# Optimization experiments

Hardware: AMD Instinct MI355X
Metric: run time of the kernel (lower is better)

The kernel has to match this reference:

```python
import jax, jax.numpy as jnp
import numpy as np
import math

D_MODEL = 2048
D_STATE = 64
D_CONV = 4
EXPAND = 2
HEADDIM = 128
NGROUPS = 1
CHUNK = 256
D_INNER = EXPAND * D_MODEL            # 4096
NHEADS = D_INNER // HEADDIM           # 32
CONV_DIM = D_INNER + 2 * NGROUPS * D_STATE   # 4224
D_IN_PROJ = 2 * D_INNER + 2 * NGROUPS * D_STATE + NHEADS  # 8352
BATCH, SEQLEN = 2, 4096
EPS = 1e-5


def segsum(x):
    # x: (..., T) -> (..., T, T) with s[i, j] = sum_{k=j+1}^{i} x[k], -inf above diag
    T = x.shape[-1]
    xx = jnp.broadcast_to(x[..., :, None], x.shape + (T,))
    mask_lo = jnp.tril(jnp.ones((T, T), dtype=bool), -1)
    xx = jnp.where(mask_lo, xx, 0.0)
    s = jnp.cumsum(xx, axis=-2)
    mask = jnp.tril(jnp.ones((T, T), dtype=bool), 0)
    return jnp.where(mask, s, -jnp.inf)


def ssd(X, A, B, C, block_len):
    # X:(b,L,h,p)  A:(b,L,h)  B,C:(b,L,h,n)
    b, L, h, p = X.shape
    c = L // block_len
    X = X.reshape(b, c, block_len, h, p)
    A = A.reshape(b, c, block_len, h).transpose(0, 3, 1, 2)  # b h c l
    B = B.reshape(b, c, block_len, h, -1)
    C = C.reshape(b, c, block_len, h, -1)
    A_cumsum = jnp.cumsum(A, axis=-1)
    Lmat = jnp.exp(segsum(A))                                  # b h c l l
    Y_diag = jnp.einsum('bclhn,bcshn,bhcls,bcshp->bclhp', C, B, Lmat, X)
    decay_states = jnp.exp(A_cumsum[:, :, :, -1:] - A_cumsum)  # b h c l
    states = jnp.einsum('bclhn,bhcl,bclhp->bchpn', B, decay_states, X)
    init = jnp.zeros_like(states[:, :1])
    states = jnp.concatenate([init, states], axis=1)
    decay_chunk = jnp.exp(segsum(jnp.pad(A_cumsum[:, :, :, -1], ((0, 0), (0, 0), (1, 0)))))
    new_states = jnp.einsum('bhzc,bchpn->bzhpn', decay_chunk, states)
    states, final_state = new_states[:, :-1], new_states[:, -1]
    Y_off = jnp.einsum('bclhn,bchpn,bhcl->bclhp', C, states, jnp.exp(A_cumsum))
    Y = (Y_diag + Y_off).reshape(b, L, h, p)
    return Y, final_state


def causal_dwconv(x, w, b):
    # x:(B,L,C)  w:(C,K) depthwise kernel  b:(C,)  -> causal conv, length preserved
    C, K = w.shape
    y = jax.lax.conv_general_dilated(
        x.transpose(0, 2, 1), w[:, None, :], (1,), [(K - 1, 0)],
        feature_group_count=C)
    return y.transpose(0, 2, 1) + b


def setup_inputs() -> dict:
    key = jax.random.key(0)
    ks = jax.random.split(key, 8)
    u = jax.random.normal(ks[0], (BATCH, SEQLEN, D_MODEL), dtype=jnp.float32)
    W_in = jax.random.normal(ks[1], (D_MODEL, D_IN_PROJ), dtype=jnp.float32) / np.sqrt(D_MODEL)
    conv_w = jax.random.normal(ks[2], (CONV_DIM, D_CONV), dtype=jnp.float32) / np.sqrt(D_CONV)
    conv_b = jnp.zeros((CONV_DIM,), dtype=jnp.float32)
    # dt_bias init: inverse-softplus of dt sampled log-uniform in [dt_min, dt_max]
    dt_min, dt_max, dt_floor = 1e-3, 1e-1, 1e-4
    dt = jnp.exp(jax.random.uniform(ks[3], (NHEADS,)) * (math.log(dt_max) - math.log(dt_min)) + math.log(dt_min))
    dt = jnp.clip(dt, dt_floor)
    dt_bias = dt + jnp.log(-jnp.expm1(-dt))
    A_log = jnp.log(jax.random.uniform(ks[4], (NHEADS,), minval=1.0, maxval=16.0))
    D = jnp.ones((NHEADS,), dtype=jnp.float32)
    norm_w = jnp.ones((D_INNER,), dtype=jnp.float32)
    W_out = jax.random.normal(ks[5], (D_INNER, D_MODEL), dtype=jnp.float32) / np.sqrt(D_INNER)
    return {"u": u, "W_in": W_in, "conv_w": conv_w, "conv_b": conv_b,
            "dt_bias": dt_bias, "A_log": A_log, "D": D, "norm_w": norm_w, "W_out": W_out}


def reference(u, W_in, conv_w, conv_b, dt_bias, A_log, D, norm_w, W_out):
    batch, seqlen, _ = u.shape
    zxbcdt = u @ W_in                                   # (B,L,8352)
    z, xBC, dt = jnp.split(zxbcdt, [D_INNER, D_INNER + CONV_DIM], axis=-1)
    dt = jax.nn.softplus(dt + dt_bias)                  # (B,L,H)
    xBC = jax.nn.silu(causal_dwconv(xBC, conv_w, conv_b))
    x, B, C = jnp.split(xBC, [D_INNER, D_INNER + NGROUPS * D_STATE], axis=-1)
    x = x.reshape(batch, seqlen, NHEADS, HEADDIM)
    B = jnp.broadcast_to(B.reshape(batch, seqlen, NGROUPS, D_STATE), (batch, seqlen, NHEADS, D_STATE))
    C = jnp.broadcast_to(C.reshape(batch, seqlen, NGROUPS, D_STATE), (batch, seqlen, NHEADS, D_STATE))
    A = -jnp.exp(A_log)                                 # (H,)
    x_scaled = x * dt[..., None]
    A_dt = A * dt                                       # (B,L,H)
    y, _final = ssd(x_scaled, A_dt, B, C, CHUNK)
    y = y.reshape(batch, seqlen, D_INNER)
    x_flat = x.reshape(batch, seqlen, D_INNER)
    D_full = jnp.repeat(D, HEADDIM)
    y = y + x_flat * D_full
    # gated RMSNorm, norm AFTER gate (norm_before_gate=False)
    yg = y * jax.nn.silu(z)
    var = jnp.mean(yg * yg, axis=-1, keepdims=True)
    y = yg * jax.lax.rsqrt(var + EPS) * norm_w
    return y @ W_out
```

## Files before the change

### kernel.cpp

```cpp
#include <hip/hip_runtime.h>

typedef short s8v __attribute__((ext_vector_type(8)));
typedef float f4v __attribute__((ext_vector_type(4)));
typedef unsigned short bfu;

#define MFMA16 __builtin_amdgcn_mfma_f32_16x16x32_bf16

constexpr int kSEQ = 4096;
constexpr int kBL  = 8192;
constexpr int kDM  = 2048;
constexpr int kDP  = 8352;
constexpr int kDPpad = 8448;
constexpr int kDI  = 4096;
constexpr int kCV  = 4224;
constexpr int kXBC = 4256;
constexpr int kNH  = 32;
constexpr int kHD  = 128;
constexpr int kDS  = 64;
constexpr int kCH  = 256;
constexpr int kLDW = 2112;
constexpr int kLDY = 4160;

#if defined(__has_builtin)
#  if __has_builtin(__builtin_amdgcn_global_load_lds)
#    define HAS_GLD 1
#  endif
#endif
#ifndef HAS_GLD
#  define HAS_GLD 0
#endif

__device__ __forceinline__ void gld_lds16(const void* g, void* lbase, int lane){
#if HAS_GLD
  (void)lane;
  __builtin_amdgcn_global_load_lds(
      (const __attribute__((address_space(1))) void*)g,
      (__attribute__((address_space(3))) void*)lbase, 16, 0, 0);
#else
  *(uint4*)((char*)lbase + lane * 16) = *(const uint4*)g;
#endif
}

__device__ __forceinline__ bfu f2bf(float f){
  union { float f; unsigned u; } c; c.f = f;
  return (bfu)((c.u + 0x7fffu + ((c.u >> 16) & 1u)) >> 16);
}
__device__ __forceinline__ float bf2f(bfu s){
  union { unsigned u; float f; } c; c.u = ((unsigned)s) << 16;
  return c.f;
}

__device__ __forceinline__ s8v frag_ld(const char* lds, int rowbase, int kh, int lane){
  int r = rowbase + (lane & 15);
  int slot = (kh << 2) + (lane >> 4);
  return *(const s8v*)(lds + (((r << 3) + (slot ^ (r & 7))) << 4));
}

__global__ __launch_bounds__(256) void k_zero(bfu* __restrict__ p, int n){
  int i = blockIdx.x * 256 + threadIdx.x;
  if (i < n) p[i] = 0;
}

__global__ __launch_bounds__(256) void k_cvt(const float* __restrict__ s, bfu* __restrict__ d, int n8){
  int i = blockIdx.x * 256 + threadIdx.x;
  int stride = gridDim.x * 256;
  for (; i < n8; i += stride){
    const float4* sp = (const float4*)(s + (size_t)i * 8);
    float4 a = sp[0], b = sp[1];
    uint4 pk; bfu* pp = (bfu*)&pk;
    pp[0]=f2bf(a.x); pp[1]=f2bf(a.y); pp[2]=f2bf(a.z); pp[3]=f2bf(a.w);
    pp[4]=f2bf(b.x); pp[5]=f2bf(b.y); pp[6]=f2bf(b.z); pp[7]=f2bf(b.w);
    *(uint4*)(d + (size_t)i * 8) = pk;
  }
}

__global__ __launch_bounds__(256) void k_transpose(const float* __restrict__ src, bfu* __restrict__ dst,
                                                   int R, int C, const float* __restrict__ scale, int ldo){
  __shared__ float tile[32][33];
  int c0 = blockIdx.x * 32, r0 = blockIdx.y * 32;
  int tx = threadIdx.x, ty = threadIdx.y;
  #pragma unroll
  for (int i = ty; i < 32; i += 8){
    int r = r0 + i, cc = c0 + tx;
    tile[i][tx] = (r < R && cc < C) ? src[(size_t)r * C + cc] : 0.f;
  }
  __syncthreads();
  #pragma unroll
  for (int i = ty; i < 32; i += 8){
    int dr = c0 + i, dc = r0 + tx;
    if (dr < C && dc < R){
      float v = tile[tx][i];
      if (scale) v *= scale[dc];
      dst[(size_t)dr * ldo + dc] = f2bf(v);
    }
  }
}

template<int MODE>
__global__ __launch_bounds__(512, 4) void k_gemm256(const bfu* __restrict__ A, const bfu* __restrict__ Bt,
                                                    float* __restrict__ outF, bfu* __restrict__ outZ,
                                                    bfu* __restrict__ outX, const float* __restrict__ rsv,
                                                    int tilesN, int N, int K, int lda, int ldb){
  extern __shared__ char lds[];
  int t = threadIdx.x, lane = t & 63, wave = t >> 6;
  int wr = wave >> 1, wc = wave & 1;
  int nwg = gridDim.x;
  int bid = blockIdx.x;
  int cpx = nwg >> 3;
  int wg = (bid & 7) * cpx + (bid >> 3);
  int bandSz = tilesN << 2;
  int band = wg / bandSz;
  int rem  = wg - band * bandSz;
  int tnTile = rem >> 2;
  int tmTile = (band << 2) + (rem & 3);
  int tm = tmTile << 8, tn = tnTile << 7;
  const bfu* Ab = A + (size_t)tm * lda;
  const bfu* Bb = Bt + (size_t)tn * ldb;

  int sr = t >> 2, scc = (t & 3) ^ ((t >> 3) & 3);
  auto stage_half = [&](const bfu* src, int ld, int ldsOfs, int kcol0){
    gld_lds16(src + (size_t)sr * ld + kcol0 + scc * 8,
              lds + ldsOfs + (wave << 10), lane);
  };
  auto stage_tile = [&](int bufOfs, int kc){
    stage_half(Ab, lda, bufOfs, kc);
    stage_half(Ab + (size_t)128 * lda, lda, bufOfs + 8192, kc);
    stage_half(Bb, ldb, bufOfs + 16384, kc);
  };
  int swz = ((lane >> 4) ^ ((lane >> 1) & 3)) << 4;

  f4v acc[4][4];
  f4v zz = {0.f, 0.f, 0.f, 0.f};
  #pragma unroll
  for (int m = 0; m < 4; ++m)
    #pragma unroll
    for (int n = 0; n < 4; ++n) acc[m][n] = zz;

  int nt = K >> 5;
  stage_tile(0, 0);
  stage_tile(24576, 32);
  __builtin_amdgcn_sched_barrier(0);
  asm volatile("s_waitcnt vmcnt(3)" ::: "memory");
  __builtin_amdgcn_sched_barrier(0);
  __builtin_amdgcn_s_barrier();
  __builtin_amdgcn_sched_barrier(0);

  int cbOfs = 0, n1Ofs = 24576, n2Ofs = 49152;
  #pragma unroll 1
  for (int tt = 0; tt < nt; ++tt){
    bool deep = (tt + 2 < nt);
    if (deep) stage_tile(n2Ofs, (tt + 2) << 5);
    s8v af[4], bf[4];
    #pragma unroll
    for (int m = 0; m < 4; ++m)
      af[m] = *(const s8v*)(lds + cbOfs + ((wr * 64 + m * 16 + (lane & 15)) << 6) + swz);
    #pragma unroll
    for (int n = 0; n < 4; ++n)
      bf[n] = *(const s8v*)(lds + cbOfs + 16384 + ((wc * 64 + n * 16 + (lane & 15)) << 6) + swz);
    __builtin_amdgcn_s_setprio(1);
    #pragma unroll
    for (int n = 0; n < 4; ++n)
      #pragma unroll
      for (int m = 0; m < 4; ++m)
        acc[m][n] = MFMA16(af[m], bf[n], acc[m][n], 0, 0, 0);
    __builtin_amdgcn_s_setprio(0);
    __builtin_amdgcn_sched_barrier(0);
    if (deep) { asm volatile("s_waitcnt vmcnt(3)" ::: "memory"); }
    else      { asm volatile("s_waitcnt vmcnt(0)" ::: "memory"); }
    __builtin_amdgcn_sched_barrier(0);
    __builtin_amdgcn_s_barrier();
    __builtin_amdgcn_sched_barrier(0);
    int tmp = cbOfs; cbOfs = n1Ofs; n1Ofs = n2Ofs; n2Ofs = tmp;
  }

  int r0 = (lane >> 4) << 2;
  if (MODE == 0){
    float* rsl = (float*)lds;
    if (t < 256) rsl[t] = rsv[tm + t];
    __syncthreads();
    #pragma unroll
    for (int m = 0; m < 4; ++m)
      #pragma unroll
      for (int n = 0; n < 4; ++n)
        #pragma unroll
        for (int r = 0; r < 4; ++r){
          int rl = wr * 64 + m * 16 + r0 + r;
          size_t rg = (size_t)(tm + rl);
          int cg = tn + wc * 64 + n * 16 + (lane & 15);
          outF[rg * N + cg] = acc[m][n][r] * rsl[rl];
        }
  } else {
    bfu* op; int ldo, cofs;
    if (tn < 4096){ op = outZ; ldo = 4096; cofs = 0; }
    else          { op = outX; ldo = kXBC; cofs = 4096; }
    #pragma unroll
    for (int h = 0; h < 2; ++h){
      __syncthreads();
      if ((wr >> 1) == h){
        #pragma unroll
        for (int m = 0; m < 4; ++m)
          #pragma unroll
          for (int n = 0; n < 4; ++n){
            int col = wc * 64 + n * 16 + (lane & 15);
            int cs = col >> 3, cl = col & 7;
            #pragma unroll
            for (int r = 0; r < 4; ++r){
              int row = (wr & 1) * 64 + m * 16 + r0 + r;
              *(bfu*)(lds + row * 256 + ((cs ^ (row & 7)) << 4) + cl * 2) = f2bf(acc[m][n][r]);
            }
          }
      }
      __syncthreads();
      int row = t >> 2;
      bfu* baseo = op + (size_t)(tm + h * 128 + row) * ldo + (tn - cofs);
      #pragma unroll
      for (int i = 0; i < 4; ++i){
        int g = (t & 3) * 4 + i;
        int cg = tn + g * 8;
        if (cg < kDP){
          uint4 v = *(const uint4*)(lds + row * 256 + ((g ^ (row & 7)) << 4));
          *(uint4*)(baseo + g * 8) = v;
        }
      }
    }
  }
}

__global__ __launch_bounds__(256) void k_conv(const bfu* __restrict__ xbc, const float* __restrict__ cw,
    const float* __restrict__ cb, bfu* __restrict__ xT,
    bfu* __restrict__ B16o, bfu* __restrict__ BTo, bfu* __restrict__ C16o){
  int cht = blockIdx.x;
  int lt = blockIdx.y;
  int b = lt >> 6;
  int l0 = (lt & 63) << 6;
  int t = threadIdx.x;
  __shared__ float w[256];
  __shared__ float bias[64];
  __shared__ bfu in16[67][66];
  __shared__ bfu out16[64][66];
  if (t < 64) bias[t] = cb[cht * 64 + t];
  w[t] = cw[cht * 256 + t];
  int chbase = cht * 64;
  for (int i = t; i < 67 * 64; i += 256){
    int rrow = i >> 6, cc = i & 63;
    int l = l0 + rrow - 3;
    bfu hv = 0;
    if (l >= 0) hv = xbc[((size_t)b * kSEQ + l) * kXBC + chbase + cc];
    in16[rrow][cc] = hv;
  }
  __syncthreads();
  for (int i = t; i < 4096; i += 256){
    int lr = i >> 6, cc = i & 63;
    float acc = bias[cc];
    #pragma unroll
    for (int j = 0; j < 4; ++j)
      acc += bf2f(in16[lr + j][cc]) * w[cc * 4 + j];
    float sv = acc / (1.f + __expf(-acc));
    out16[lr][cc] = f2bf(sv);
  }
  __syncthreads();
  if (chbase >= 4096){
    for (int i = t; i < 4096; i += 256){
      int lr = i >> 6, cc = i & 63;
      size_t row = (size_t)b * kSEQ + l0 + lr;
      int ch = chbase + cc;
      bfu v = out16[lr][cc];
      if (ch < 4096 + kDS) B16o[row * kDS + (ch - 4096)] = v;
      else                 C16o[row * kDS + (ch - 4096 - kDS)] = v;
    }
  }
  if (chbase < 4096 + kDS){
    for (int i = t; i < 4096; i += 256){
      int cc = i >> 6, lr = i & 63;
      int ch = chbase + cc;
      int lg = l0 + lr;
      bfu v = out16[lr][cc];
      if (ch < 4096){
        int hh = ch >> 7, p = ch & 127;
        xT[(((size_t)b * kNH + hh) * kHD + p) * kSEQ + lg] = v;
      } else if (ch < 4096 + kDS){
        BTo[((size_t)b * kDS + (ch - 4096)) * kSEQ + lg] = v;
      }
    }
  }
}

__global__ __launch_bounds__(256) void k_dtscan(const bfu* __restrict__ xbc, const float* __restrict__ dt_bias,
    const float* __restrict__ A_log, float* __restrict__ dtf, float* __restrict__ acum){
  int bi = blockIdx.x;
  int h = bi & 31, c = (bi >> 5) & 15, b = bi >> 9;
  int t = threadIdx.x;
  size_t row = (size_t)b * kSEQ + c * kCH + t;
  float draw = bf2f(xbc[row * kXBC + kCV + h]) + dt_bias[h];
  float dt = (draw > 20.f) ? draw : log1pf(__expf(draw));
  dtf[row * kNH + h] = dt;
  float dA = -__expf(A_log[h]) * dt;
  __shared__ float s[256];
  s[t] = dA;
  __syncthreads();
  #pragma unroll
  for (int off = 1; off < 256; off <<= 1){
    float v = (t >= off) ? s[t - off] : 0.f;
    __syncthreads();
    s[t] += v;
    __syncthreads();
  }
  acum[(size_t)bi * 256 + t] = s[t];
}

__global__ __launch_bounds__(256) void k_states(const bfu* __restrict__ xT, const bfu* __restrict__ BT,
    const float* __restrict__ dtf, const float* __restrict__ acum, bfu* __restrict__ states){
  int bi = blockIdx.x;
  int h = bi & 31, c = (bi >> 5) & 15, b = bi >> 9;
  int t = threadIdx.x, lane = t & 63, wave = t >> 6;
  int wr = wave >> 1, wc = wave & 1;
  __shared__ uint4 ldsX4[1024];
  __shared__ uint4 ldsB4[512];
  __shared__ float dsv[256];
  char* ldsX = (char*)ldsX4;
  char* ldsB = (char*)ldsB4;
  float Atot = acum[(size_t)bi * 256 + 255];
  {
    size_t row = (size_t)b * kSEQ + c * kCH + t;
    dsv[t] = dtf[row * kNH + h] * __expf(Atot - acum[(size_t)bi * 256 + t]);
  }
  f4v zz = {0.f, 0.f, 0.f, 0.f};
  f4v acc[4][2];
  #pragma unroll
  for (int m = 0; m < 4; ++m){ acc[m][0] = zz; acc[m][1] = zz; }
  const bfu* xTp = xT + ((size_t)b * kNH + h) * kHD * kSEQ + c * kCH;
  const bfu* BTp = BT + (size_t)b * kDS * kSEQ + c * kCH;
  __syncthreads();
  for (int kb = 0; kb < 4; ++kb){
    #pragma unroll
    for (int it = 0; it < 4; ++it){
      int s = it * 256 + t;
      int row = s >> 3;
      int srcslot = (s & 7) ^ (row & 7);
      gld_lds16(xTp + (size_t)row * kSEQ + kb * 64 + srcslot * 8,
                ldsX + it * 4096 + wave * 1024, lane);
    }
    #pragma unroll
    for (int it = 0; it < 2; ++it){
      int cidx = it * 256 + t;
      int row = cidx >> 3, slot = cidx & 7;
      uint4 v = *(const uint4*)(BTp + (size_t)row * kSEQ + kb * 64 + slot * 8);
      bfu* hp = (bfu*)&v;
      #pragma unroll
      for (int j = 0; j < 8; ++j)
        hp[j] = f2bf(bf2f(hp[j]) * dsv[kb * 64 + slot * 8 + j]);
      *(uint4*)(ldsB + (((row << 3) + (slot ^ (row & 7))) << 4)) = v;
    }
    __syncthreads();
    s8v af[4][2], bb[2][2];
    #pragma unroll
    for (int m = 0; m < 4; ++m){
      af[m][0] = frag_ld(ldsX, wr * 64 + m * 16, 0, lane);
      af[m][1] = frag_ld(ldsX, wr * 64 + m * 16, 1, lane);
    }
    #pragma unroll
    for (int nf = 0; nf < 2; ++nf){
      bb[nf][0] = frag_ld(ldsB, wc * 32 + nf * 16, 0, lane);
      bb[nf][1] = frag_ld(ldsB, wc * 32 + nf * 16, 1, lane);
    }
    #pragma unroll
    for (int kh = 0; kh < 2; ++kh)
      #pragma unroll
      for (int m = 0; m < 4; ++m)
        #pragma unroll
        for (int nf = 0; nf < 2; ++nf)
          acc[m][nf] = MFMA16(af[m][kh], bb[nf][kh], acc[m][nf], 0, 0, 0);
    __syncthreads();
  }
  bfu* sp = states + (size_t)bi * 8192;
  int r0 = (lane >> 4) << 2;
  #pragma unroll
  for (int m = 0; m < 4; ++m)
    #pragma unroll
    for (int nf = 0; nf < 2; ++nf)
      #pragma unroll
      for (int r = 0; r < 4; ++r){
        int p = wr * 64 + m * 16 + r0 + r;
        int n = wc * 32 + nf * 16 + (lane & 15);
        sp[p * 64 + n] = f2bf(acc[m][nf][r]);
      }
}

__global__ __launch_bounds__(256) void k_scan(bfu* __restrict__ st, const float* __restrict__ acum){
  int bh = blockIdx.x >> 2;
  int jg = blockIdx.x & 3;
  int b = bh >> 5, h = bh & 31;
  int t = threadIdx.x;
  float run[8];
  #pragma unroll
  for (int j = 0; j < 8; ++j) run[j] = 0.f;
  for (int c = 0; c < 16; ++c){
    size_t bi = (size_t)((b * 16 + c) * 32 + h);
    float eT = __expf(acum[bi * 256 + 255]);
    size_t base = bi * 8192 + (size_t)jg * 2048;
    #pragma unroll
    for (int j = 0; j < 8; ++j){
      size_t idx = base + j * 256 + t;
      float sl = bf2f(st[idx]);
      st[idx] = f2bf(run[j]);
      run[j] = run[j] * eT + sl;
    }
  }
}

__global__ __launch_bounds__(256) void k_y(
    const bfu* __restrict__ xT, const bfu* __restrict__ Bm, const bfu* __restrict__ Cm,
    const bfu* __restrict__ SIs, const float* __restrict__ dtf, const float* __restrict__ acum,
    const bfu* __restrict__ z16, const float* __restrict__ Dp,
    bfu* __restrict__ y16)
{
  int bi = blockIdx.x;
  int h = bi & 31, c = (bi >> 5) & 15, b = bi >> 9;
  int ph = blockIdx.y;
  int t = threadIdx.x, lane = t & 63, wave = t >> 6;
  int wl = wave << 6;
  __shared__ uint4 ldsP4[2048];
  __shared__ uint4 ldsT4[512];
  __shared__ float acumS[256];
  __shared__ float dtS[256];
  char* ldsP = ((char*)ldsP4) + (wave << 13);
  char* ldsT = (char*)ldsT4;
  size_t rowbase = (size_t)b * kSEQ + c * kCH;
  acumS[t] = acum[(size_t)bi * 256 + t];
  dtS[t] = dtf[(rowbase + t) * kNH + h];
  const bfu* SIp = SIs + (size_t)bi * 8192 + (size_t)ph * 4096;
  #pragma unroll
  for (int it = 0; it < 2; ++it){
    int cidx = it * 256 + t;
    int row = cidx >> 3, slot = cidx & 7;
    uint4 v = *(const uint4*)(SIp + row * 64 + slot * 8);
    *(uint4*)(ldsT + (((row << 3) + (slot ^ (row & 7))) << 4)) = v;
  }
  const bfu* Cp = Cm + rowbase * kDS;
  s8v cf[4][2];
  #pragma unroll
  for (int m = 0; m < 4; ++m){
    cf[m][0] = *(const s8v*)(Cp + (size_t)(wl + m * 16 + (lane & 15)) * kDS + ((lane >> 4) << 3));
    cf[m][1] = *(const s8v*)(Cp + (size_t)(wl + m * 16 + (lane & 15)) * kDS + 32 + ((lane >> 4) << 3));
  }
  __syncthreads();
  float Arow[16];
  #pragma unroll
  for (int m = 0; m < 4; ++m)
    #pragma unroll
    for (int r = 0; r < 4; ++r)
      Arow[m * 4 + r] = acumS[wl + m * 16 + ((lane >> 4) << 2) + r];
  f4v acc[4][4];
  {
    s8v bfo[4][2];
    #pragma unroll
    for (int pf = 0; pf < 4; ++pf){
      bfo[pf][0] = frag_ld(ldsT, pf << 4, 0, lane);
      bfo[pf][1] = frag_ld(ldsT, pf << 4, 1, lane);
    }
    f4v zz = {0.f, 0.f, 0.f, 0.f};
    #pragma unroll
    for (int m = 0; m < 4; ++m)
      #pragma unroll
      for (int pf = 0; pf < 4; ++pf){
        f4v v = zz;
        v = MFMA16(cf[m][0], bfo[pf][0], v, 0, 0, 0);
        v = MFMA16(cf[m][1], bfo[pf][1], v, 0, 0, 0);
        #pragma unroll
        for (int r = 0; r < 4; ++r) v[r] *= __expf(Arow[m * 4 + r]);
        acc[m][pf] = v;
      }
  }
  float Dh = Dp[h];
  const bfu* Bp = Bm + rowbase * kDS;
  const bfu* xTp = xT + (((size_t)b * kNH + h) * kHD + ph * 64) * kSEQ + c * kCH;
  #pragma unroll 1
  for (int sb = 0; sb < 4; ++sb){
    __syncthreads();
    #pragma unroll
    for (int it = 0; it < 2; ++it){
      int s = it * 256 + t;
      int row = s >> 3;
      int srcslot = (s & 7) ^ (row & 7);
      gld_lds16(xTp + (size_t)row * kSEQ + sb * 64 + srcslot * 8,
                ldsT + it * 4096 + wave * 1024, lane);
    }
    f4v sv[4][4];
    {
      s8v bsf[4][2];
      #pragma unroll
      for (int sf = 0; sf < 4; ++sf){
        bsf[sf][0] = *(const s8v*)(Bp + (size_t)(sb * 64 + sf * 16 + (lane & 15)) * kDS + ((lane >> 4) << 3));
        bsf[sf][1] = *(const s8v*)(Bp + (size_t)(sb * 64 + sf * 16 + (lane & 15)) * kDS + 32 + ((lane >> 4) << 3));
      }
      f4v zz = {0.f, 0.f, 0.f, 0.f};
      #pragma unroll
      for (int m = 0; m < 4; ++m)
        #pragma unroll
        for (int sf = 0; sf < 4; ++sf){
          f4v v = zz;
          v = MFMA16(cf[m][0], bsf[sf][0], v, 0, 0, 0);
          v = MFMA16(cf[m][1], bsf[sf][1], v, 0, 0, 0);
          sv[m][sf] = v;
        }
    }
    int scb = sb << 6;
    float As[4], dts_[4];
    #pragma unroll
    for (int sf = 0; sf < 4; ++sf){
      As[sf] = acumS[scb + sf * 16 + (lane & 15)];
      dts_[sf] = dtS[scb + sf * 16 + (lane & 15)];
    }
    #pragma unroll
    for (int m = 0; m < 4; ++m)
      #pragma unroll
      for (int sf = 0; sf < 4; ++sf)
        #pragma unroll
        for (int r = 0; r < 4; ++r){
          int rloc = m * 16 + ((lane >> 4) << 2) + r;
          int scl = sf * 16 + (lane & 15);
          int d = (wl + rloc) - (scb + scl);
          float pv = 0.f;
          if (d >= 0)
            pv = sv[m][sf][r] * __expf(Arow[m * 4 + r] - As[sf]) * dts_[sf];
          if (d == 0)
            pv += Dh;
          *(bfu*)(ldsP + rloc * 128 + ((((scl >> 3) ^ (rloc & 7)) << 3) + (scl & 7)) * 2) = f2bf(pv);
        }
    __syncthreads();
    s8v xb[4][2];
    #pragma unroll
    for (int pf = 0; pf < 4; ++pf){
      xb[pf][0] = frag_ld(ldsT, pf << 4, 0, lane);
      xb[pf][1] = frag_ld(ldsT, pf << 4, 1, lane);
    }
    #pragma unroll
    for (int m = 0; m < 4; ++m){
      s8v pa0 = frag_ld(ldsP, m << 4, 0, lane);
      s8v pa1 = frag_ld(ldsP, m << 4, 1, lane);
      #pragma unroll
      for (int pf = 0; pf < 4; ++pf){
        acc[m][pf] = MFMA16(pa0, xb[pf][0], acc[m][pf], 0, 0, 0);
        acc[m][pf] = MFMA16(pa1, xb[pf][1], acc[m][pf], 0, 0, 0);
      }
    }
  }
  __syncthreads();
  char* ldsY = (char*)ldsP4;
  #pragma unroll
  for (int m = 0; m < 4; ++m)
    #pragma unroll
    for (int pf = 0; pf < 4; ++pf)
      #pragma unroll
      for (int r = 0; r < 4; ++r){
        int rloc = wl + m * 16 + ((lane >> 4) << 2) + r;
        int col  = (pf << 4) + (lane & 15);
        *(bfu*)(ldsY + rloc * 128 + (((col >> 3) ^ (rloc & 7)) << 4) + (col & 7) * 2) = f2bf(acc[m][pf][r]);
      }
  __syncthreads();
  int cg0 = (h << 7) + (ph << 6);
  #pragma unroll
  for (int j = 0; j < 8; ++j){
    int idx = j * 256 + t;
    int row = idx >> 3, g = idx & 7;
    uint4 yv = *(const uint4*)(ldsY + row * 128 + ((g ^ (row & 7)) << 4));
    size_t rowg = rowbase + row;
    uint4 zv4 = *(const uint4*)(z16 + rowg * kDI + cg0 + g * 8);
    const bfu* yp = (const bfu*)&yv;
    const bfu* zp = (const bfu*)&zv4;
    uint4 out; bfu* op = (bfu*)&out;
    #pragma unroll
    for (int e = 0; e < 8; ++e){
      float zv = bf2f(zp[e]);
      float sg = zv / (1.f + __expf(-zv));
      op[e] = f2bf(bf2f(yp[e]) * sg);
    }
    *(uint4*)(y16 + rowg * kLDY + cg0 + g * 8) = out;
  }
}

__global__ __launch_bounds__(256) void k_rms(const bfu* __restrict__ y, float* __restrict__ rs){
  int row = blockIdx.x;
  int t = threadIdx.x, lane = t & 63, wave = t >> 6;
  const bfu* yp = y + (size_t)row * kLDY;
  uint4 a = *(const uint4*)(yp + t * 8);
  uint4 b = *(const uint4*)(yp + 2048 + t * 8);
  const bfu* ap = (const bfu*)&a;
  const bfu* bp = (const bfu*)&b;
  float ss = 0.f;
  #pragma unroll
  for (int j = 0; j < 8; ++j){
    float va = bf2f(ap[j]); ss += va * va;
    float vb = bf2f(bp[j]); ss += vb * vb;
  }
  #pragma unroll
  for (int o = 32; o > 0; o >>= 1) ss += __shfl_down(ss, o, 64);
  __shared__ float red[4];
  if (lane == 0) red[wave] = ss;
  __syncthreads();
  if (t == 0){
    float tot = red[0] + red[1] + red[2] + red[3];
    rs[row] = rsqrtf(tot * (1.f / 4096.f) + 1e-5f);
  }
}

extern "C" void kernel_launch(void* const* d_in, const int* in_sizes, int n_in,
                              void* d_out, int out_size, void* d_ws, size_t ws_size,
                              hipStream_t stream){
  (void)in_sizes; (void)n_in; (void)out_size; (void)ws_size;
  const float* u       = (const float*)d_in[0];
  const float* W_in    = (const float*)d_in[1];
  const float* conv_w  = (const float*)d_in[2];
  const float* conv_b  = (const float*)d_in[3];
  const float* dt_bias = (const float*)d_in[4];
  const float* A_log   = (const float*)d_in[5];
  const float* Dp      = (const float*)d_in[6];
  const float* norm_w  = (const float*)d_in[7];
  const float* W_out   = (const float*)d_in[8];
  char* ws = (char*)d_ws;

  const size_t o_z    = 0;
  const size_t o_xbc  = o_z   + (size_t)kBL * kDI * 2;
  const size_t o_u16  = o_xbc + (size_t)kBL * kXBC * 2;
  const size_t o_xT   = o_u16 + (size_t)kBL * kDM * 2;
  const size_t o_B16  = o_xT  + (size_t)kBL * kDI * 2;
  const size_t o_BT   = o_B16 + (size_t)kBL * kDS * 2;
  const size_t o_C16  = o_BT  + (size_t)kBL * kDS * 2;
  const size_t o_dtf  = o_C16 + (size_t)kBL * kDS * 2;
  const size_t o_acum = o_dtf + (size_t)kBL * kNH * 4;
  const size_t o_rs   = o_acum + (size_t)1024 * 256 * 4;
  const size_t o_states = o_u16;
  const size_t o_woutT  = o_u16 + (size_t)1024 * 8192 * 2;
  const size_t o_winT   = o_xT;
  const size_t o_y16    = o_xbc;

  bfu* z16    = (bfu*)(ws + o_z);
  bfu* xbc    = (bfu*)(ws + o_xbc);
  bfu* u16    = (bfu*)(ws + o_u16);
  bfu* xT     = (bfu*)(ws + o_xT);
  bfu* B16    = (bfu*)(ws + o_B16);
  bfu* BT     = (bfu*)(ws + o_BT);
  bfu* C16    = (bfu*)(ws + o_C16);
  float* dtf  = (float*)(ws + o_dtf);
  float* acum = (float*)(ws + o_acum);
  float* rs   = (float*)(ws + o_rs);
  bfu* statesS= (bfu*)(ws + o_states);
  bfu* woutT  = (bfu*)(ws + o_woutT);
  bfu* winT   = (bfu*)(ws + o_winT);
  bfu* y16    = (bfu*)(ws + o_y16);

  (void)hipFuncSetAttribute(reinterpret_cast<const void*>(&k_gemm256<2>),
                            hipFuncAttributeMaxDynamicSharedMemorySize, 73728);
  (void)hipFuncSetAttribute(reinterpret_cast<const void*>(&k_gemm256<0>),
                            hipFuncAttributeMaxDynamicSharedMemorySize, 73728);

  k_zero<<<(96 * kLDW + 255) / 256, 256, 0, stream>>>(winT + (size_t)kDP * kLDW, 96 * kLDW);
  k_cvt<<<2048, 256, 0, stream>>>(u, u16, kBL * kDM / 8);
  k_transpose<<<dim3(kDP / 32, kDM / 32), dim3(32, 8), 0, stream>>>(W_in, winT, kDM, kDP, nullptr, kLDW);
  k_gemm256<2><<<(kDPpad / 128) * (kBL / 256), 512, 73728, stream>>>(u16, winT, nullptr, z16, xbc, nullptr, kDPpad / 128, kDPpad, kDM, kDM, kLDW);
  k_conv<<<dim3(kCV / 64, kBL / 64), 256, 0, stream>>>(xbc, conv_w, conv_b, xT, B16, BT, C16);
  k_dtscan<<<1024, 256, 0, stream>>>(xbc, dt_bias, A_log, dtf, acum);
  k_transpose<<<dim3(kDM / 32, kDI / 32), dim3(32, 8), 0, stream>>>(W_out, woutT, kDI, kDM, norm_w, kDI);
  k_states<<<1024, 256, 0, stream>>>(xT, BT, dtf, acum, statesS);
  k_scan<<<256, 256, 0, stream>>>(statesS, acum);
  k_y<<<dim3(1024, 2), 256, 0, stream>>>(xT, B16, C16, statesS, dtf, acum, z16, Dp, y16);
  k_rms<<<kBL, 256, 0, stream>>>(y16, rs);
  k_gemm256<0><<<(kDM / 128) * (kBL / 256), 512, 73728, stream>>>(y16, woutT, (float*)d_out, nullptr, nullptr, rs, kDM / 128, kDM, kDI, kLDY, kDI);
}
```

Measured before the change: 835.9 us.

## Merge the two head-dim halves of k_y into one 512-thread block sharing the P matrix

k_y previously ran two blocks per (batch, chunk, head), one per 64-wide half of the head dimension, and each recomputed the full C·B^T score matrix P. Now a single 512-thread block handles both halves. The eight waves split the P computation (32 rows each) and write it to shared LDS, and each group of four waves then multiplies P by its own half of x. This halves the redundant CB MFMAs, the exp work and the B/C loads. In exchange the block uses more LDS and registers, and the epilogue is serialized into two halves with extra barriers.

```diff
diff --git a/kernel.cpp b/kernel.cpp
--- a/kernel.cpp
+++ b/kernel.cpp
@@ -408,7 +408,7 @@
   }
 }
 
-__global__ __launch_bounds__(256) void k_y(
+__global__ __launch_bounds__(512, 2) void k_y(
     const bfu* __restrict__ xT, const bfu* __restrict__ Bm, const bfu* __restrict__ Cm,
     const bfu* __restrict__ SIs, const float* __restrict__ dtf, const float* __restrict__ acum,
     const bfu* __restrict__ z16, const float* __restrict__ Dp,
@@ -416,40 +416,55 @@
 {
   int bi = blockIdx.x;
   int h = bi & 31, c = (bi >> 5) & 15, b = bi >> 9;
-  int ph = blockIdx.y;
   int t = threadIdx.x, lane = t & 63, wave = t >> 6;
-  int wl = wave << 6;
+  int rw = wave & 3;
+  int pg = wave >> 2;
+  int tl = rw * 64 + lane;
   __shared__ uint4 ldsP4[2048];
-  __shared__ uint4 ldsT4[512];
+  __shared__ uint4 ldsT4[1024];
   __shared__ float acumS[256];
   __shared__ float dtS[256];
-  char* ldsP = ((char*)ldsP4) + (wave << 13);
-  char* ldsT = (char*)ldsT4;
+  char* ldsP = (char*)ldsP4;
+  char* ldsT = ((char*)ldsT4) + pg * 8192;
   size_t rowbase = (size_t)b * kSEQ + c * kCH;
-  acumS[t] = acum[(size_t)bi * 256 + t];
-  dtS[t] = dtf[(rowbase + t) * kNH + h];
-  const bfu* SIp = SIs + (size_t)bi * 8192 + (size_t)ph * 4096;
+  if (t < 256){
+    acumS[t] = acum[(size_t)bi * 256 + t];
+    dtS[t] = dtf[(rowbase + t) * kNH + h];
+  }
+  const bfu* SIp = SIs + (size_t)bi * 8192 + (size_t)pg * 4096;
   #pragma unroll
   for (int it = 0; it < 2; ++it){
-    int cidx = it * 256 + t;
+    int cidx = it * 256 + tl;
     int row = cidx >> 3, slot = cidx & 7;
     uint4 v = *(const uint4*)(SIp + row * 64 + slot * 8);
     *(uint4*)(ldsT + (((row << 3) + (slot ^ (row & 7))) << 4)) = v;
   }
   const bfu* Cp = Cm + rowbase * kDS;
-  s8v cf[4][2];
+  s8v cfP[4][2];
   #pragma unroll
   for (int m = 0; m < 4; ++m){
-    cf[m][0] = *(const s8v*)(Cp + (size_t)(wl + m * 16 + (lane & 15)) * kDS + ((lane >> 4) << 3));
-    cf[m][1] = *(const s8v*)(Cp + (size_t)(wl + m * 16 + (lane & 15)) * kDS + 32 + ((lane >> 4) << 3));
+    cfP[m][0] = *(const s8v*)(Cp + (size_t)(rw * 64 + m * 16 + (lane & 15)) * kDS + ((lane >> 4) << 3));
+    cfP[m][1] = *(const s8v*)(Cp + (size_t)(rw * 64 + m * 16 + (lane & 15)) * kDS + 32 + ((lane >> 4) << 3));
+  }
+  s8v cfS[2][2];
+  #pragma unroll
+  for (int m = 0; m < 2; ++m){
+    cfS[m][0] = *(const s8v*)(Cp + (size_t)(wave * 32 + m * 16 + (lane & 15)) * kDS + ((lane >> 4) << 3));
+    cfS[m][1] = *(const s8v*)(Cp + (size_t)(wave * 32 + m * 16 + (lane & 15)) * kDS + 32 + ((lane >> 4) << 3));
   }
   __syncthreads();
-  float Arow[16];
+  float ArowP[16];
   #pragma unroll
   for (int m = 0; m < 4; ++m)
     #pragma unroll
     for (int r = 0; r < 4; ++r)
-      Arow[m * 4 + r] = acumS[wl + m * 16 + ((lane >> 4) << 2) + r];
+      ArowP[m * 4 + r] = acumS[rw * 64 + m * 16 + ((lane >> 4) << 2) + r];
+  float ArowS[8];
+  #pragma unroll
+  for (int m = 0; m < 2; ++m)
+    #pragma unroll
+    for (int r = 0; r < 4; ++r)
+      ArowS[m * 4 + r] = acumS[wave * 32 + m * 16 + ((lane >> 4) << 2) + r];
   f4v acc[4][4];
   {
     s8v bfo[4][2];
@@ -464,28 +479,28 @@
       #pragma unroll
       for (int pf = 0; pf < 4; ++pf){
         f4v v = zz;
-        v = MFMA16(cf[m][0], bfo[pf][0], v, 0, 0, 0);
-        v = MFMA16(cf[m][1], bfo[pf][1], v, 0, 0, 0);
+        v = MFMA16(cfP[m][0], bfo[pf][0], v, 0, 0, 0);
+        v = MFMA16(cfP[m][1], bfo[pf][1], v, 0, 0, 0);
         #pragma unroll
-        for (int r = 0; r < 4; ++r) v[r] *= __expf(Arow[m * 4 + r]);
+        for (int r = 0; r < 4; ++r) v[r] *= __expf(ArowP[m * 4 + r]);
         acc[m][pf] = v;
       }
   }
   float Dh = Dp[h];
   const bfu* Bp = Bm + rowbase * kDS;
-  const bfu* xTp = xT + (((size_t)b * kNH + h) * kHD + ph * 64) * kSEQ + c * kCH;
+  const bfu* xTp = xT + (((size_t)b * kNH + h) * kHD + pg * 64) * kSEQ + c * kCH;
   #pragma unroll 1
   for (int sb = 0; sb < 4; ++sb){
     __syncthreads();
     #pragma unroll
     for (int it = 0; it < 2; ++it){
-      int s = it * 256 + t;
+      int s = it * 256 + tl;
       int row = s >> 3;
       int srcslot = (s & 7) ^ (row & 7);
       gld_lds16(xTp + (size_t)row * kSEQ + sb * 64 + srcslot * 8,
-                ldsT + it * 4096 + wave * 1024, lane);
-    }
-    f4v sv[4][4];
+                ldsT + it * 4096 + rw * 1024, lane);
+    }
+    f4v sv[2][4];
     {
       s8v bsf[4][2];
       #pragma unroll
@@ -495,12 +510,12 @@
       }
       f4v zz = {0.f, 0.f, 0.f, 0.f};
       #pragma unroll
-      for (int m = 0; m < 4; ++m)
+      for (int m = 0; m < 2; ++m)
         #pragma unroll
         for (int sf = 0; sf < 4; ++sf){
           f4v v = zz;
-          v = MFMA16(cf[m][0], bsf[sf][0], v, 0, 0, 0);
-          v = MFMA16(cf[m][1], bsf[sf][1], v, 0, 0, 0);
+          v = MFMA16(cfS[m][0], bsf[sf][0], v, 0, 0, 0);
+          v = MFMA16(cfS[m][1], bsf[sf][1], v, 0, 0, 0);
           sv[m][sf] = v;
         }
     }
@@ -512,20 +527,20 @@
       dts_[sf] = dtS[scb + sf * 16 + (lane & 15)];
     }
     #pragma unroll
-    for (int m = 0; m < 4; ++m)
+    for (int m = 0; m < 2; ++m)
       #pragma unroll
       for (int sf = 0; sf < 4; ++sf)
         #pragma unroll
         for (int r = 0; r < 4; ++r){
-          int rloc = m * 16 + ((lane >> 4) << 2) + r;
+          int pr = wave * 32 + m * 16 + ((lane >> 4) << 2) + r;
           int scl = sf * 16 + (lane & 15);
-          int d = (wl + rloc) - (scb + scl);
+          int d = pr - (scb + scl);
           float pv = 0.f;
           if (d >= 0)
-            pv = sv[m][sf][r] * __expf(Arow[m * 4 + r] - As[sf]) * dts_[sf];
+            pv = sv[m][sf][r] * __expf(ArowS[m * 4 + r] - As[sf]) * dts_[sf];
           if (d == 0)
             pv += Dh;
-          *(bfu*)(ldsP + rloc * 128 + ((((scl >> 3) ^ (rloc & 7)) << 3) + (scl & 7)) * 2) = f2bf(pv);
+          *(bfu*)(ldsP + pr * 128 + ((((scl >> 3) ^ (pr & 7)) << 3) + (scl & 7)) * 2) = f2bf(pv);
         }
     __syncthreads();
     s8v xb[4][2];
@@ -536,8 +551,8 @@
     }
     #pragma unroll
     for (int m = 0; m < 4; ++m){
-      s8v pa0 = frag_ld(ldsP, m << 4, 0, lane);
-      s8v pa1 = frag_ld(ldsP, m << 4, 1, lane);
+      s8v pa0 = frag_ld(ldsP, rw * 64 + m * 16, 0, lane);
+      s8v pa1 = frag_ld(ldsP, rw * 64 + m * 16, 1, lane);
       #pragma unroll
       for (int pf = 0; pf < 4; ++pf){
         acc[m][pf] = MFMA16(pa0, xb[pf][0], acc[m][pf], 0, 0, 0);
@@ -545,37 +560,42 @@
       }
     }
   }
-  __syncthreads();
   char* ldsY = (char*)ldsP4;
   #pragma unroll
-  for (int m = 0; m < 4; ++m)
-    #pragma unroll
-    for (int pf = 0; pf < 4; ++pf)
-      #pragma unroll
-      for (int r = 0; r < 4; ++r){
-        int rloc = wl + m * 16 + ((lane >> 4) << 2) + r;
-        int col  = (pf << 4) + (lane & 15);
-        *(bfu*)(ldsY + rloc * 128 + (((col >> 3) ^ (rloc & 7)) << 4) + (col & 7) * 2) = f2bf(acc[m][pf][r]);
-      }
-  __syncthreads();
-  int cg0 = (h << 7) + (ph << 6);
-  #pragma unroll
-  for (int j = 0; j < 8; ++j){
-    int idx = j * 256 + t;
-    int row = idx >> 3, g = idx & 7;
-    uint4 yv = *(const uint4*)(ldsY + row * 128 + ((g ^ (row & 7)) << 4));
-    size_t rowg = rowbase + row;
-    uint4 zv4 = *(const uint4*)(z16 + rowg * kDI + cg0 + g * 8);
-    const bfu* yp = (const bfu*)&yv;
-    const bfu* zp = (const bfu*)&zv4;
-    uint4 out; bfu* op = (bfu*)&out;
-    #pragma unroll
-    for (int e = 0; e < 8; ++e){
-      float zv = bf2f(zp[e]);
-      float sg = zv / (1.f + __expf(-zv));
-      op[e] = f2bf(bf2f(yp[e]) * sg);
-    }
-    *(uint4*)(y16 + rowg * kLDY + cg0 + g * 8) = out;
+  for (int half = 0; half < 2; ++half){
+    __syncthreads();
+    if (pg == half){
+      #pragma unroll
+      for (int m = 0; m < 4; ++m)
+        #pragma unroll
+        for (int pf = 0; pf < 4; ++pf)
+          #pragma unroll
+          for (int r = 0; r < 4; ++r){
+            int rloc = rw * 64 + m * 16 + ((lane >> 4) << 2) + r;
+            int col  = (pf << 4) + (lane & 15);
+            *(bfu*)(ldsY + rloc * 128 + (((col >> 3) ^ (rloc & 7)) << 4) + (col & 7) * 2) = f2bf(acc[m][pf][r]);
+          }
+    }
+    __syncthreads();
+    int cg0 = (h << 7) + (half << 6);
+    #pragma unroll
+    for (int j = 0; j < 4; ++j){
+      int idx = j * 512 + t;
+      int row = idx >> 3, g = idx & 7;
+      uint4 yv = *(const uint4*)(ldsY + row * 128 + ((g ^ (row & 7)) << 4));
+      size_t rowg = rowbase + row;
+      uint4 zv4 = *(const uint4*)(z16 + rowg * kDI + cg0 + g * 8);
+      const bfu* yp = (const bfu*)&yv;
+      const bfu* zp = (const bfu*)&zv4;
+      uint4 outv; bfu* op = (bfu*)&outv;
+      #pragma unroll
+      for (int e = 0; e < 8; ++e){
+        float zv = bf2f(zp[e]);
+        float sg = zv / (1.f + __expf(-zv));
+        op[e] = f2bf(bf2f(yp[e]) * sg);
+      }
+      *(uint4*)(y16 + rowg * kLDY + cg0 + g * 8) = outv;
+    }
   }
 }
 
@@ -663,7 +683,7 @@
   k_transpose<<<dim3(kDM / 32, kDI / 32), dim3(32, 8), 0, stream>>>(W_out, woutT, kDI, kDM, norm_w, kDI);
   k_states<<<1024, 256, 0, stream>>>(xT, BT, dtf, acum, statesS);
   k_scan<<<256, 256, 0, stream>>>(statesS, acum);
-  k_y<<<dim3(1024, 2), 256, 0, stream>>>(xT, B16, C16, statesS, dtf, acum, z16, Dp, y16);
+  k_y<<<1024, 512, 0, stream>>>(xT, B16, C16, statesS, dtf, acum, z16, Dp, y16);
   k_rms<<<kBL, 256, 0, stream>>>(y16, rs);
   k_gemm256<0><<<(kDM / 128) * (kBL / 256), 512, 73728, stream>>>(y16, woutT, (float*)d_out, nullptr, nullptr, rs, kDM / 128, kDM, kDI, kLDY, kDI);
 }
```

Result: faster. 740.3 us (-11.4%).
